# Kernel optimization log

Measured on AMD Instinct MI355X. Metric: run time of the kernel, lower is better.

The kernel has to match this reference:

```python
import jax, jax.numpy as jnp
import numpy as np

LN_EPS = 1e-12  # BERT LayerNorm eps


def _lstm_dir(x, wih, whh, bih, bhh, reverse):
    # x: [T, B, D] -> outputs [T, B, Hd]; torch gate order i, f, g, o
    B = x.shape[1]
    Hd = whh.shape[1]
    b = bih + bhh

    def step(carry, xt):
        h, c = carry
        gates = xt @ wih.T + h @ whh.T + b  # [B, 4*Hd]
        i, f, g, o = jnp.split(gates, 4, axis=-1)
        c = jax.nn.sigmoid(f) * c + jax.nn.sigmoid(i) * jnp.tanh(g)
        h = jax.nn.sigmoid(o) * jnp.tanh(c)
        return (h, c), h

    init = (jnp.zeros((B, Hd), x.dtype), jnp.zeros((B, Hd), x.dtype))
    _, ys = jax.lax.scan(step, init, x, reverse=reverse)
    return ys


def _forward(input_ids, labels, word_emb, pos_emb, type_emb, ln_g, ln_b,
             w_ih, w_hh, b_ih, b_hh, fc_w, fc_b, crf_start, crf_end, crf_trans):
    B, T = input_ids.shape
    # BERT embeddings (eval mode: dropout = identity)
    emb = word_emb[input_ids] + pos_emb[:T][None, :, :] + type_emb[0][None, None, :]
    mu = emb.mean(-1, keepdims=True)
    var = ((emb - mu) ** 2).mean(-1, keepdims=True)
    emb = (emb - mu) / jnp.sqrt(var + LN_EPS) * ln_g + ln_b

    # stacked bidirectional LSTM
    x = emb.transpose(1, 0, 2)  # [T, B, 768]
    n_layers = w_ih.shape[0]
    for l in range(n_layers):
        f = _lstm_dir(x, w_ih[l, 0], w_hh[l, 0], b_ih[l, 0], b_hh[l, 0], False)
        r = _lstm_dir(x, w_ih[l, 1], w_hh[l, 1], b_ih[l, 1], b_hh[l, 1], True)
        x = jnp.concatenate([f, r], axis=-1)  # [T, B, 768]
    out = x.transpose(1, 0, 2)  # [B, T, 768]

    em = out @ fc_w.T + fc_b  # emissions [B, T, C]

    # CRF log-likelihood (full mask, torchcrf reduction='sum')
    gold_em = jnp.take_along_axis(em, labels[..., None], axis=2)[..., 0]  # [B, T]
    score = (crf_start[labels[:, 0]]
             + gold_em.sum(axis=1)
             + crf_trans[labels[:, :-1], labels[:, 1:]].sum(axis=1)
             + crf_end[labels[:, -1]])

    alpha0 = crf_start[None, :] + em[:, 0]  # [B, C]

    def step(alpha, e_t):
        a = jax.nn.logsumexp(alpha[:, :, None] + crf_trans[None, :, :], axis=1) + e_t
        return a, None

    alpha, _ = jax.lax.scan(step, alpha0, em[:, 1:].transpose(1, 0, 2))
    logZ = jax.nn.logsumexp(alpha + crf_end[None, :], axis=1)  # [B]
    return jnp.sum(logZ - score)  # loss = -llh


def setup_inputs() -> dict:
    key = jax.random.key(0)
    ks = jax.random.split(key, 16)
    B, T, V, P, D, C, L, Hd = 32, 256, 30522, 512, 768, 14, 2, 384
    s = 0.05
    return {
        "input_ids": jax.random.randint(ks[0], (B, T), 0, V),
        "labels": jax.random.randint(ks[1], (B, T), 0, C),
        "word_emb": jax.random.normal(ks[2], (V, D), jnp.float32) * 0.02,
        "pos_emb": jax.random.normal(ks[3], (P, D), jnp.float32) * 0.02,
        "type_emb": jax.random.normal(ks[4], (2, D), jnp.float32) * 0.02,
        "ln_g": jnp.ones((D,), jnp.float32),
        "ln_b": jnp.zeros((D,), jnp.float32),
        "w_ih": jax.random.normal(ks[5], (L, 2, 4 * Hd, D), jnp.float32) * s,
        "w_hh": jax.random.normal(ks[6], (L, 2, 4 * Hd, Hd), jnp.float32) * s,
        "b_ih": jax.random.normal(ks[7], (L, 2, 4 * Hd), jnp.float32) * s,
        "b_hh": jax.random.normal(ks[8], (L, 2, 4 * Hd), jnp.float32) * s,
        "fc_w": jax.random.normal(ks[9], (C, D), jnp.float32) * s,
        "fc_b": jnp.zeros((C,), jnp.float32),
        "crf_start": jax.random.normal(ks[10], (C,), jnp.float32) * 0.1,
        "crf_end": jax.random.normal(ks[11], (C,), jnp.float32) * 0.1,
        "crf_trans": jax.random.normal(ks[12], (C, C), jnp.float32) * 0.1,
    }


def reference(input_ids, labels, word_emb, pos_emb, type_emb, ln_g, ln_b,
              w_ih, w_hh, b_ih, b_hh, fc_w, fc_b, crf_start, crf_end, crf_trans):
    return _forward(input_ids, labels, word_emb, pos_emb, type_emb, ln_g, ln_b,
                    w_ih, w_hh, b_ih, b_hh, fc_w, fc_b, crf_start, crf_end, crf_trans)
```

## Files before the change

### kernel.cpp

```cpp
#include <hip/hip_runtime.h>

typedef unsigned short u16;
typedef unsigned long long u64;
typedef __bf16 bfx8 __attribute__((ext_vector_type(8)));
typedef float  fx4  __attribute__((ext_vector_type(4)));

static __device__ __forceinline__ float b2f(u16 u){
  unsigned v = ((unsigned)u) << 16;
  return __builtin_bit_cast(float, v);
}
static __device__ __forceinline__ u16 f2b(float f){
  unsigned u = __builtin_bit_cast(unsigned, f);
  u = (u + 0x7FFFu + ((u >> 16) & 1u)) >> 16;
  return (u16)u;
}
static __device__ __forceinline__ float blo(unsigned v){ return b2f((u16)(v & 0xFFFFu)); }
static __device__ __forceinline__ float bhi(unsigned v){ return b2f((u16)(v >> 16)); }
static __device__ __forceinline__ float sigm(float x){
  float cx = fminf(fmaxf(x, -30.f), 30.f);
  float e = __expf(-cx);
  return __builtin_amdgcn_rcpf(1.f + e);
}
static __device__ __forceinline__ float tanh_f(float x){
  float cx = fminf(fmaxf(x, -15.f), 15.f);
  float e = __expf(2.f * cx);
  return (e - 1.f) * __builtin_amdgcn_rcpf(e + 1.f);
}
static __device__ __forceinline__ u64 ald64(const u64* p){
  return __hip_atomic_load(p, __ATOMIC_RELAXED, __HIP_MEMORY_SCOPE_AGENT);
}
static __device__ __forceinline__ void ast64(u64* p, u64 v){
  __hip_atomic_store(p, v, __ATOMIC_RELAXED, __HIP_MEMORY_SCOPE_AGENT);
}

__global__ __launch_bounds__(256) void embed_ln(
    const int* __restrict__ ids, const float* __restrict__ we,
    const float* __restrict__ pe, const float* __restrict__ te,
    const float* __restrict__ lng, const float* __restrict__ lnb,
    u16* __restrict__ X)
{
  int row = blockIdx.x;
  int t = row >> 5, b = row & 31;
  int id = ids[b * 256 + t];
  int tid = threadIdx.x;
  int wv = tid >> 6, lane = tid & 63;
  __shared__ float red[8];
  float v[3]; float s = 0.f, s2 = 0.f;
  const float* wrow = we + (long)id * 768;
  const float* prow = pe + (long)t * 768;
#pragma unroll
  for (int u = 0; u < 3; ++u){
    int k = tid + 256 * u;
    float x = wrow[k] + prow[k] + te[k];
    v[u] = x; s += x; s2 += x * x;
  }
#pragma unroll
  for (int o = 32; o > 0; o >>= 1){ s += __shfl_xor(s, o); s2 += __shfl_xor(s2, o); }
  if (lane == 0){ red[wv] = s; red[4 + wv] = s2; }
  __syncthreads();
  float S  = red[0] + red[1] + red[2] + red[3];
  float S2 = red[4] + red[5] + red[6] + red[7];
  float mu = S * (1.f / 768.f);
  float var = S2 * (1.f / 768.f) - mu * mu;
  float rs = rsqrtf(var + 1e-12f);
#pragma unroll
  for (int u = 0; u < 3; ++u){
    int k = tid + 256 * u;
    float y = (v[u] - mu) * rs * lng[k] + lnb[k];
    X[(long)row * 768 + k] = f2b(y);
  }
}

__global__ __launch_bounds__(256) void conv_wih(
    const float* __restrict__ w, u16* __restrict__ o)
{
  long i = ((long)blockIdx.x * 256 + threadIdx.x) * 4;
  float4 v = *reinterpret_cast<const float4*>(&w[i]);
  short4 pk;
  pk.x = (short)f2b(v.x); pk.y = (short)f2b(v.y);
  pk.z = (short)f2b(v.z); pk.w = (short)f2b(v.w);
  *reinterpret_cast<short4*>(&o[i]) = pk;
}

__global__ __launch_bounds__(256) void gemm_pre(
    const u16* __restrict__ A,
    const u16* __restrict__ W,
    const float* __restrict__ bi,
    const float* __restrict__ bh,
    u16* __restrict__ pre)
{
  __shared__ u16 la[64][40];
  __shared__ u16 lb[64][40];
  int m0 = blockIdx.x * 64, n0 = blockIdx.y * 64;
  int tid = threadIdx.x;
  int wv = tid >> 6, lane = tid & 63;
  int l15 = lane & 15, l4 = lane >> 4;
  int r = tid >> 2, seg = (tid & 3) * 8;
  fx4 acc[4];
#pragma unroll
  for (int i = 0; i < 4; ++i){ acc[i][0]=0.f; acc[i][1]=0.f; acc[i][2]=0.f; acc[i][3]=0.f; }
  for (int k0 = 0; k0 < 768; k0 += 32){
    __syncthreads();
    *reinterpret_cast<uint4*>(&la[r][seg]) =
        *reinterpret_cast<const uint4*>(&A[(long)(m0 + r) * 768 + k0 + seg]);
    *reinterpret_cast<uint4*>(&lb[r][seg]) =
        *reinterpret_cast<const uint4*>(&W[(long)(n0 + r) * 768 + k0 + seg]);
    __syncthreads();
    bfx8 af = __builtin_bit_cast(bfx8, *reinterpret_cast<const uint4*>(&la[wv * 16 + l15][8 * l4]));
#pragma unroll
    for (int nt = 0; nt < 4; ++nt){
      bfx8 bf = __builtin_bit_cast(bfx8, *reinterpret_cast<const uint4*>(&lb[nt * 16 + l15][8 * l4]));
      acc[nt] = __builtin_amdgcn_mfma_f32_16x16x32_bf16(af, bf, acc[nt], 0, 0, 0);
    }
  }
#pragma unroll
  for (int nt = 0; nt < 4; ++nt){
    int n = n0 + nt * 16 + l15;
    int d = (n >= 1536) ? 1 : 0;
    int np = n - d * 1536;
    float bias = bi[n] + bh[n];
#pragma unroll
    for (int q = 0; q < 4; ++q){
      int m = m0 + wv * 16 + 4 * l4 + q;
      int tt = m >> 5, bb = m & 31;
      float vv = acc[nt][q] + bias;
      pre[((long)((d * 256 + tt) * 32 + bb)) * 1536 + np] = f2b(vv);
    }
  }
}

__global__ __launch_bounds__(256) void lstm_layer(
    const float* __restrict__ Whh,
    const u16*  __restrict__ pre,
    u16* __restrict__ Y,
    u64* __restrict__ H64)
{
  __shared__ u16 lw[64][386];
  __shared__ u16 hb[32][386];
  __shared__ float gl2[4][16][33];
  int wg = blockIdx.x;
  int d = wg / 24, sl = wg - d * 24;
  int js = sl * 16;
  int tid = threadIdx.x;
  int wv = tid >> 6, lane = tid & 63;
  int l15 = lane & 15, l4 = lane >> 4;
  int b0 = tid & 31, q = tid >> 5;
  int jl0 = 2 * q, jl1 = 2 * q + 1;

  ast64(&H64[((long)(1 * 2 + d) * 192 + sl * 8 + q) * 32 + b0], 0ull);
  u64 own_word = 0ull;

  for (int i = tid; i < 64 * 96; i += 256){
    int rr = i / 96, c4 = i - rr * 96;
    const float* src = Whh + ((long)(d * 1536 + (rr >> 4) * 384 + js + (rr & 15))) * 384 + 4 * c4;
    float4 v = *reinterpret_cast<const float4*>(src);
    short4 pk;
    pk.x = (short)f2b(v.x); pk.y = (short)f2b(v.y);
    pk.z = (short)f2b(v.z); pk.w = (short)f2b(v.w);
    *reinterpret_cast<short4*>(&lw[rr][(4 * c4) ^ (8 * (rr & 7))]) = pk;
  }
  __syncthreads();

  float c0 = 0.f, c1 = 0.f;

  int t0 = d ? 255 : 0;
  int t1 = d ? 254 : 1;
  const u16* pb0 = pre + ((long)(d * 256 + t0) * 32 + b0) * 1536 + js + jl0;
  const u16* pb1 = pre + ((long)(d * 256 + t1) * 32 + b0) * 1536 + js + jl0;
  uint4 pc, pn;
  pc.x = *reinterpret_cast<const unsigned*>(pb0 + 0 * 384);
  pc.y = *reinterpret_cast<const unsigned*>(pb0 + 1 * 384);
  pc.z = *reinterpret_cast<const unsigned*>(pb0 + 2 * 384);
  pc.w = *reinterpret_cast<const unsigned*>(pb0 + 3 * 384);
  pn.x = *reinterpret_cast<const unsigned*>(pb1 + 0 * 384);
  pn.y = *reinterpret_cast<const unsigned*>(pb1 + 1 * 384);
  pn.z = *reinterpret_cast<const unsigned*>(pb1 + 2 * 384);
  pn.w = *reinterpret_cast<const unsigned*>(pb1 + 3 * 384);

  for (int s = 0; s < 256; ++s){
    int tt = d ? (255 - s) : s;
    int pr = (s + 1) & 1;
    int pw = s & 1;

    {
      const u64* hsrc = H64 + (long)(pr * 2 + d) * 192 * 32;
      unsigned tagv = (unsigned)s;
      __builtin_amdgcn_s_sleep(2);
      for (;;){
        u64 vb[24];
#pragma unroll
        for (int i = 0; i < 24; ++i) vb[i] = ald64(&hsrc[tid + 256 * i]);
#pragma unroll
        for (int i = 0; i < 24; ++i) if (i == sl) vb[i] = own_word;
        bool ok = true;
#pragma unroll
        for (int i = 0; i < 24; ++i) ok = ok && ((unsigned)(vb[i] >> 32) == tagv);
#pragma unroll
        for (int i = 0; i < 24; ++i){
          int f = tid + 256 * i;
          int bb = f & 31, j2 = f >> 5;
          *reinterpret_cast<unsigned*>(&hb[bb][(2 * j2) ^ (8 * (bb & 7))]) = (unsigned)vb[i];
        }
        if (__syncthreads_and((int)ok)) break;
      }
    }

    int s2 = (s + 2 < 256) ? (s + 2) : 255;
    int t2 = d ? (255 - s2) : s2;
    const u16* pb2 = pre + ((long)(d * 256 + t2) * 32 + b0) * 1536 + js + jl0;
    uint4 p2;
    p2.x = *reinterpret_cast<const unsigned*>(pb2 + 0 * 384);
    p2.y = *reinterpret_cast<const unsigned*>(pb2 + 1 * 384);
    p2.z = *reinterpret_cast<const unsigned*>(pb2 + 2 * 384);
    p2.w = *reinterpret_cast<const unsigned*>(pb2 + 3 * 384);

    fx4 a0a, a0b, a1a, a1b;
#pragma unroll
    for (int z = 0; z < 4; ++z){ a0a[z]=0.f; a0b[z]=0.f; a1a[z]=0.f; a1b[z]=0.f; }
#pragma unroll
    for (int kk = 0; kk < 12; kk += 2){
      int col0 = (kk * 32 + 8 * l4) ^ (8 * (l15 & 7));
      int col1 = ((kk + 1) * 32 + 8 * l4) ^ (8 * (l15 & 7));
      bfx8 bw0 = __builtin_bit_cast(bfx8, *reinterpret_cast<const uint4*>(&lw[wv * 16 + l15][col0]));
      bfx8 h00 = __builtin_bit_cast(bfx8, *reinterpret_cast<const uint4*>(&hb[l15][col0]));
      bfx8 h10 = __builtin_bit_cast(bfx8, *reinterpret_cast<const uint4*>(&hb[16 + l15][col0]));
      bfx8 bw1 = __builtin_bit_cast(bfx8, *reinterpret_cast<const uint4*>(&lw[wv * 16 + l15][col1]));
      bfx8 h01 = __builtin_bit_cast(bfx8, *reinterpret_cast<const uint4*>(&hb[l15][col1]));
      bfx8 h11 = __builtin_bit_cast(bfx8, *reinterpret_cast<const uint4*>(&hb[16 + l15][col1]));
      a0a = __builtin_amdgcn_mfma_f32_16x16x32_bf16(h00, bw0, a0a, 0, 0, 0);
      a1a = __builtin_amdgcn_mfma_f32_16x16x32_bf16(h10, bw0, a1a, 0, 0, 0);
      a0b = __builtin_amdgcn_mfma_f32_16x16x32_bf16(h01, bw1, a0b, 0, 0, 0);
      a1b = __builtin_amdgcn_mfma_f32_16x16x32_bf16(h11, bw1, a1b, 0, 0, 0);
    }
#pragma unroll
    for (int qq = 0; qq < 4; ++qq){
      int bb0 = (4 * l4 + qq) ^ (4 * (l15 & 7));
      int bb1 = (16 + 4 * l4 + qq) ^ (4 * (l15 & 7));
      gl2[wv][l15][bb0] = a0a[qq] + a0b[qq];
      gl2[wv][l15][bb1] = a1a[qq] + a1b[qq];
    }
    __syncthreads();

    int x0 = b0 ^ (4 * (jl0 & 7));
    int x1 = b0 ^ (4 * (jl1 & 7));
    float gi0 = gl2[0][jl0][x0] + blo(pc.x), gi1 = gl2[0][jl1][x1] + bhi(pc.x);
    float gf0 = gl2[1][jl0][x0] + blo(pc.y), gf1 = gl2[1][jl1][x1] + bhi(pc.y);
    float gg0 = gl2[2][jl0][x0] + blo(pc.z), gg1 = gl2[2][jl1][x1] + bhi(pc.z);
    float go0 = gl2[3][jl0][x0] + blo(pc.w), go1 = gl2[3][jl1][x1] + bhi(pc.w);
    c0 = sigm(gf0) * c0 + sigm(gi0) * tanh_f(gg0);
    float h0 = sigm(go0) * tanh_f(c0);
    c1 = sigm(gf1) * c1 + sigm(gi1) * tanh_f(gg1);
    float h1 = sigm(go1) * tanh_f(c1);

    unsigned hv = (unsigned)f2b(h0) | ((unsigned)f2b(h1) << 16);
    own_word = ((u64)(unsigned)(s + 1) << 32) | (u64)hv;
    ast64(&H64[((long)(pw * 2 + d) * 192 + sl * 8 + q) * 32 + b0], own_word);
    *reinterpret_cast<unsigned*>(&Y[((long)tt * 32 + b0) * 768 + d * 384 + js + jl0]) = hv;
    pc = pn; pn = p2;
  }
}

__global__ __launch_bounds__(256) void fc_em(
    const u16* __restrict__ Y2, const float* __restrict__ fw,
    const float* __restrict__ fb, float* __restrict__ em)
{
  int row = blockIdx.x * 4 + (threadIdx.x >> 6);
  int lane = threadIdx.x & 63;
  float acc[14];
#pragma unroll
  for (int c = 0; c < 14; ++c) acc[c] = 0.f;
#pragma unroll
  for (int u = 0; u < 6; ++u){
    int k2 = (lane + 64 * u) * 2;
    unsigned yv = *reinterpret_cast<const unsigned*>(&Y2[(long)row * 768 + k2]);
    float y0 = blo(yv), y1 = bhi(yv);
#pragma unroll
    for (int c = 0; c < 14; ++c){
      float2 f = *reinterpret_cast<const float2*>(&fw[c * 768 + k2]);
      acc[c] += y0 * f.x + y1 * f.y;
    }
  }
#pragma unroll
  for (int c = 0; c < 14; ++c){
    float a = acc[c];
#pragma unroll
    for (int o = 32; o > 0; o >>= 1) a += __shfl_xor(a, o);
    acc[c] = a;
  }
  if (lane == 0){
    int tt = row >> 5, b = row & 31;
#pragma unroll
    for (int c = 0; c < 14; ++c) em[(long)(b * 256 + tt) * 14 + c] = acc[c] + fb[c];
  }
}

__global__ __launch_bounds__(64) void crf_fwd(
    const float* __restrict__ em,
    const int* __restrict__ labels,
    const float* __restrict__ cs, const float* __restrict__ ce,
    const float* __restrict__ ct,
    float* __restrict__ lossb)
{
  int b = blockIdx.x;
  int lane = threadIdx.x;
  const float* E = em + (long)b * 256 * 14;
  const int* L = labels + b * 256;

  float sc = 0.f;
  for (int t = lane; t < 256; t += 64){
    int lt = L[t];
    sc += E[t * 14 + lt];
    if (t < 255) sc += ct[lt * 14 + L[t + 1]];
  }
#pragma unroll
  for (int o = 32; o > 0; o >>= 1) sc += __shfl_xor(sc, o);
  float score = sc + cs[L[0]] + ce[L[255]];

  __shared__ float al[2][16];
  int j = lane >> 2, ih = lane & 3;
  if (lane < 16){
    al[0][lane] = (lane < 14) ? (cs[lane] + E[lane]) : -1e30f;
    al[1][lane] = -1e30f;
  }
  __syncthreads();
  float tr[4];
#pragma unroll
  for (int w = 0; w < 4; ++w){
    int i = ih * 4 + w;
    tr[w] = (i < 14 && j < 14) ? ct[i * 14 + j] : -1e30f;
  }
  for (int t = 1; t < 256; ++t){
    int par = t & 1;
    float vals[4]; float m = -1e30f;
#pragma unroll
    for (int w = 0; w < 4; ++w){
      int i = ih * 4 + w;
      float v = al[par ^ 1][i] + tr[w];
      vals[w] = v; m = fmaxf(m, v);
    }
    m = fmaxf(m, __shfl_xor(m, 1));
    m = fmaxf(m, __shfl_xor(m, 2));
    float s = 0.f;
#pragma unroll
    for (int w = 0; w < 4; ++w) s += __expf(vals[w] - m);
    s += __shfl_xor(s, 1);
    s += __shfl_xor(s, 2);
    if (ih == 0 && j < 14) al[par][j] = m + __logf(s) + E[t * 14 + j];
    __syncthreads();
  }
  float v = (lane < 14) ? (al[1][lane] + ce[lane]) : -1e30f;
  float mm = v;
#pragma unroll
  for (int o = 32; o > 0; o >>= 1) mm = fmaxf(mm, __shfl_xor(mm, o));
  float ss = (lane < 14) ? __expf(v - mm) : 0.f;
#pragma unroll
  for (int o = 32; o > 0; o >>= 1) ss += __shfl_xor(ss, o);
  if (lane == 0) lossb[b] = (mm + __logf(ss)) - score;
}

__global__ __launch_bounds__(64) void final_sum(const float* __restrict__ lb, float* __restrict__ out){
  int lane = threadIdx.x;
  float v = (lane < 32) ? lb[lane] : 0.f;
#pragma unroll
  for (int o = 32; o > 0; o >>= 1) v += __shfl_xor(v, o);
  if (lane == 0) out[0] = v;
}

extern "C" void kernel_launch(void* const* d_in, const int* in_sizes, int n_in,
                              void* d_out, int out_size, void* d_ws, size_t ws_size,
                              hipStream_t stream)
{
  const int*   ids = (const int*)d_in[0];
  const int*   lab = (const int*)d_in[1];
  const float* we  = (const float*)d_in[2];
  const float* pe  = (const float*)d_in[3];
  const float* te  = (const float*)d_in[4];
  const float* lng = (const float*)d_in[5];
  const float* lnb = (const float*)d_in[6];
  const float* wih = (const float*)d_in[7];
  const float* whh = (const float*)d_in[8];
  const float* bih = (const float*)d_in[9];
  const float* bhh = (const float*)d_in[10];
  const float* fcw = (const float*)d_in[11];
  const float* fcb = (const float*)d_in[12];
  const float* cs  = (const float*)d_in[13];
  const float* ce  = (const float*)d_in[14];
  const float* ct  = (const float*)d_in[15];
  float* out = (float*)d_out;

  char* ws = (char*)d_ws;
  size_t off = 0;
  u16* X0  = (u16*)(ws + off); off += (size_t)8192 * 768 * 2;
  u16* Y1  = (u16*)(ws + off); off += (size_t)8192 * 768 * 2;
  u16* PRE = (u16*)(ws + off); off += (size_t)2 * 256 * 32 * 1536 * 2;
  float* EM = (float*)(ws + off); off += (size_t)32 * 256 * 14 * 4;
  u64* H64a = (u64*)(ws + off); off += (size_t)2 * 2 * 192 * 32 * 8;
  u64* H64b = (u64*)(ws + off); off += (size_t)2 * 2 * 192 * 32 * 8;
  u16* WIHB = (u16*)(ws + off); off += (size_t)2 * 2 * 1536 * 768 * 2;
  float* LB = (float*)(ws + off); off += 128;
  u16* Y2 = X0;

  conv_wih<<<4608, 256, 0, stream>>>(wih, WIHB);
  embed_ln<<<8192, 256, 0, stream>>>(ids, we, pe, te, lng, lnb, X0);

  gemm_pre<<<dim3(128, 48), 256, 0, stream>>>(X0, WIHB, bih, bhh, PRE);
  lstm_layer<<<48, 256, 0, stream>>>(whh, PRE, Y1, H64a);
  gemm_pre<<<dim3(128, 48), 256, 0, stream>>>(Y1, WIHB + (size_t)2 * 1536 * 768,
                                              bih + 2 * 1536, bhh + 2 * 1536, PRE);
  lstm_layer<<<48, 256, 0, stream>>>(whh + (size_t)2 * 1536 * 384, PRE, Y2, H64b);

  fc_em<<<2048, 256, 0, stream>>>(Y2, fcw, fcb, EM);
  crf_fwd<<<32, 64, 0, stream>>>(EM, lab, cs, ce, ct, LB);
  final_sum<<<1, 64, 0, stream>>>(LB, out);
}
```

Before: 2.389 ms.

## Enlarge input-projection GEMM tiles to 128x128 with direct global-to-LDS loads

The input-projection GEMM moves from 64x64 tiles, where each wave computed a 16x64 strip, to 128x128 tiles with a 4x4 grid of MFMA accumulators per wave. This raises operand reuse from LDS and cuts global traffic per FLOP. Tiles are now staged with global_load_lds, which copies straight into LDS without passing through registers, and the padded LDS layout is dropped. The trade-offs are more accumulator registers, possible LDS bank conflicts from the unpadded layout, and fewer blocks (1536 instead of 6144). The GEMM is likely a small part of the total time next to the sequential LSTM kernels.

```diff
diff --git a/kernel.cpp b/kernel.cpp
--- a/kernel.cpp
+++ b/kernel.cpp
@@ -31,6 +31,11 @@
 }
 static __device__ __forceinline__ void ast64(u64* p, u64 v){
   __hip_atomic_store(p, v, __ATOMIC_RELAXED, __HIP_MEMORY_SCOPE_AGENT);
+}
+static __device__ __forceinline__ void gload_lds16(const void* g, void* l){
+  __builtin_amdgcn_global_load_lds(
+      (const __attribute__((address_space(1))) void*)(g),
+      (__attribute__((address_space(3))) void*)(l), 16, 0, 0);
 }
 
 __global__ __launch_bounds__(256) void embed_ln(
@@ -89,42 +94,67 @@
     const float* __restrict__ bh,
     u16* __restrict__ pre)
 {
-  __shared__ u16 la[64][40];
-  __shared__ u16 lb[64][40];
-  int m0 = blockIdx.x * 64, n0 = blockIdx.y * 64;
+  __shared__ u16 la[128 * 32];
+  __shared__ u16 lb[128 * 32];
+  int m0 = blockIdx.x * 128, n0 = blockIdx.y * 128;
   int tid = threadIdx.x;
   int wv = tid >> 6, lane = tid & 63;
   int l15 = lane & 15, l4 = lane >> 4;
-  int r = tid >> 2, seg = (tid & 3) * 8;
-  fx4 acc[4];
-#pragma unroll
-  for (int i = 0; i < 4; ++i){ acc[i][0]=0.f; acc[i][1]=0.f; acc[i][2]=0.f; acc[i][3]=0.f; }
+  int wr = (wv >> 1) * 64, wc = (wv & 1) * 64;
+  int srow = lane >> 2;
+  int scol = 8 * (lane & 3);
+
+  fx4 acc[4][4];
+#pragma unroll
+  for (int mi = 0; mi < 4; ++mi)
+#pragma unroll
+    for (int ni = 0; ni < 4; ++ni){
+      acc[mi][ni][0]=0.f; acc[mi][ni][1]=0.f; acc[mi][ni][2]=0.f; acc[mi][ni][3]=0.f;
+    }
+
   for (int k0 = 0; k0 < 768; k0 += 32){
     __syncthreads();
-    *reinterpret_cast<uint4*>(&la[r][seg]) =
-        *reinterpret_cast<const uint4*>(&A[(long)(m0 + r) * 768 + k0 + seg]);
-    *reinterpret_cast<uint4*>(&lb[r][seg]) =
-        *reinterpret_cast<const uint4*>(&W[(long)(n0 + r) * 768 + k0 + seg]);
+#pragma unroll
+    for (int r = 0; r < 2; ++r){
+      int blk = r * 4 + wv;
+      gload_lds16(A + (long)(m0 + blk * 16 + srow) * 768 + k0 + scol,
+                  &la[blk * 512]);
+      gload_lds16(W + (long)(n0 + blk * 16 + srow) * 768 + k0 + scol,
+                  &lb[blk * 512]);
+    }
     __syncthreads();
-    bfx8 af = __builtin_bit_cast(bfx8, *reinterpret_cast<const uint4*>(&la[wv * 16 + l15][8 * l4]));
-#pragma unroll
-    for (int nt = 0; nt < 4; ++nt){
-      bfx8 bf = __builtin_bit_cast(bfx8, *reinterpret_cast<const uint4*>(&lb[nt * 16 + l15][8 * l4]));
-      acc[nt] = __builtin_amdgcn_mfma_f32_16x16x32_bf16(af, bf, acc[nt], 0, 0, 0);
-    }
-  }
-#pragma unroll
-  for (int nt = 0; nt < 4; ++nt){
-    int n = n0 + nt * 16 + l15;
+
+    bfx8 af[4], bf[4];
+#pragma unroll
+    for (int mi = 0; mi < 4; ++mi)
+      af[mi] = __builtin_bit_cast(bfx8,
+        *reinterpret_cast<const uint4*>(&la[(wr + mi * 16 + l15) * 32 + 8 * l4]));
+#pragma unroll
+    for (int ni = 0; ni < 4; ++ni)
+      bf[ni] = __builtin_bit_cast(bfx8,
+        *reinterpret_cast<const uint4*>(&lb[(wc + ni * 16 + l15) * 32 + 8 * l4]));
+#pragma unroll
+    for (int mi = 0; mi < 4; ++mi)
+#pragma unroll
+      for (int ni = 0; ni < 4; ++ni)
+        acc[mi][ni] = __builtin_amdgcn_mfma_f32_16x16x32_bf16(af[mi], bf[ni], acc[mi][ni], 0, 0, 0);
+  }
+
+#pragma unroll
+  for (int ni = 0; ni < 4; ++ni){
+    int n = n0 + wc + ni * 16 + l15;
     int d = (n >= 1536) ? 1 : 0;
     int np = n - d * 1536;
     float bias = bi[n] + bh[n];
 #pragma unroll
-    for (int q = 0; q < 4; ++q){
-      int m = m0 + wv * 16 + 4 * l4 + q;
-      int tt = m >> 5, bb = m & 31;
-      float vv = acc[nt][q] + bias;
-      pre[((long)((d * 256 + tt) * 32 + bb)) * 1536 + np] = f2b(vv);
+    for (int mi = 0; mi < 4; ++mi){
+#pragma unroll
+      for (int q = 0; q < 4; ++q){
+        int m = m0 + wr + mi * 16 + 4 * l4 + q;
+        int tt = m >> 5, bb = m & 31;
+        float vv = acc[mi][ni][q] + bias;
+        pre[((long)((d * 256 + tt) * 32 + bb)) * 1536 + np] = f2b(vv);
+      }
     }
   }
 }
@@ -403,10 +433,10 @@
   conv_wih<<<4608, 256, 0, stream>>>(wih, WIHB);
   embed_ln<<<8192, 256, 0, stream>>>(ids, we, pe, te, lng, lnb, X0);
 
-  gemm_pre<<<dim3(128, 48), 256, 0, stream>>>(X0, WIHB, bih, bhh, PRE);
+  gemm_pre<<<dim3(64, 24), 256, 0, stream>>>(X0, WIHB, bih, bhh, PRE);
   lstm_layer<<<48, 256, 0, stream>>>(whh, PRE, Y1, H64a);
-  gemm_pre<<<dim3(128, 48), 256, 0, stream>>>(Y1, WIHB + (size_t)2 * 1536 * 768,
-                                              bih + 2 * 1536, bhh + 2 * 1536, PRE);
+  gemm_pre<<<dim3(64, 24), 256, 0, stream>>>(Y1, WIHB + (size_t)2 * 1536 * 768,
+                                             bih + 2 * 1536, bhh + 2 * 1536, PRE);
   lstm_layer<<<48, 256, 0, stream>>>(whh + (size_t)2 * 1536 * 384, PRE, Y2, H64b);
 
   fc_em<<<2048, 256, 0, stream>>>(Y2, fcw, fcb, EM);
```

Result: faster. 2.316 ms (-3.0%).
